# Optimization experiments

Hardware: AMD Instinct MI355X
Metric: run time of the kernel (lower is better)

## Reference

```python
import jax, jax.numpy as jnp
import numpy as np

B, T, L, D = 512, 100, 256, 128
DEPTH = 8                 # perfect binary tree depth -> path length DEPTH+1
P = DEPTH + 1
N_PER_TREE = 2 * L - 1    # 511 nodes per tree (heap layout)
N_TOTAL = T * N_PER_TREE  # 51100 global nodes


def _build_paths():
    # Heap layout per tree: internal nodes 0..L-2, leaves L-1..2L-2.
    # Path for leaf l = chain of heap ancestors from root to leaf.
    local = np.zeros((L, P), dtype=np.int32)
    for l in range(L):
        node = L - 1 + l
        chain = []
        while True:
            chain.append(node)
            if node == 0:
                break
            node = (node - 1) // 2
        local[l] = np.array(chain[::-1], dtype=np.int32)
    offs = (np.arange(T, dtype=np.int32) * N_PER_TREE)[:, None, None]
    return local[None, :, :] + offs  # [T, L, P] global node ids


def setup_inputs() -> dict:
    key = jax.random.key(0)
    k1, k2, k3, k4, k5, k6 = jax.random.split(key, 6)
    paths = jnp.asarray(_build_paths())
    # GBDT multi-hot: exactly one activated leaf per tree per sample
    leaf = jax.random.randint(k1, (B, T), 0, L)
    cross = (jnp.zeros((B, T, L), jnp.float32)
             .at[jnp.arange(B)[:, None], jnp.arange(T)[None, :], leaf]
             .set(1.0)
             .reshape(B, T * L))
    s = 1.0 / float(np.sqrt(D))  # torch LSTM init range
    node_emb = jax.random.normal(k2, (N_TOTAL, D), jnp.float32) * 0.01
    w_ih = jax.random.uniform(k3, (4 * D, D), jnp.float32, -s, s)
    w_hh = jax.random.uniform(k4, (4 * D, D), jnp.float32, -s, s)
    b_ih = jax.random.uniform(k5, (4 * D,), jnp.float32, -s, s)
    b_hh = jax.random.uniform(k6, (4 * D,), jnp.float32, -s, s)
    return {"cross_features": cross, "node_emb": node_emb, "w_ih": w_ih,
            "w_hh": w_hh, "b_ih": b_ih, "b_hh": b_hh, "paths": paths}


def _lstm_last_h(x, w_ih, w_hh, b_ih, b_hh):
    # x: [S, P, D] -> final hidden state [S, D]; torch gate order i, f, g, o
    S = x.shape[0]
    d = w_hh.shape[1]
    bias = b_ih + b_hh

    def step(carry, x_t):
        h, c = carry
        g = x_t @ w_ih.T + h @ w_hh.T + bias          # [S, 4D]
        i, f, gg, o = jnp.split(g, 4, axis=-1)
        c = jax.nn.sigmoid(f) * c + jax.nn.sigmoid(i) * jnp.tanh(gg)
        h = jax.nn.sigmoid(o) * jnp.tanh(c)
        return (h, c), None

    h0 = jnp.zeros((S, d), x.dtype)
    (h, _), _ = jax.lax.scan(step, (h0, h0), jnp.swapaxes(x, 0, 1))
    return h


def reference(cross_features, node_emb, w_ih, w_hh, b_ih, b_hh, paths):
    t, l, p = paths.shape
    b = cross_features.shape[0]
    d = node_emb.shape[1]
    cf = cross_features.reshape(b, t, l)
    leaf = jnp.argmax(cf, axis=-1)                    # [B, T] activated leaf per tree
    active = jnp.any(cf > 0, axis=-1)                 # [B, T] tree has an activated leaf
    node_ids = paths[jnp.arange(t)[None, :], leaf]    # [B, T, P] root-to-leaf global ids
    x = node_emb[node_ids].reshape(b * t, p, d)       # batched path gather
    h = _lstm_last_h(x, w_ih, w_hh, b_ih, b_hh).reshape(b, t, d)
    return jnp.where(active[..., None], h, jnp.zeros((), h.dtype))
```

## Files before the change

kernel.cpp:

```cpp
#include <hip/hip_runtime.h>
#include <math.h>


#define B_N 512
#define T_N 100
#define L_N 256
#define D_N 128
#define NPT 511

typedef __attribute__((ext_vector_type(8))) short short8;
typedef __attribute__((ext_vector_type(4))) float f32x4;
typedef __attribute__((ext_vector_type(4))) unsigned short ushort4v;

__device__ __forceinline__ unsigned short f2bf(float f) {
    unsigned u = __float_as_uint(f);
    return (unsigned short)((u + 0x7FFFu + ((u >> 16) & 1u)) >> 16);
}
__device__ __forceinline__ float bf2f(unsigned short b) {
    return __uint_as_float(((unsigned)b) << 16);
}
__device__ __forceinline__ float fsigmoid(float x) {
    return __builtin_amdgcn_rcpf(1.f + __builtin_amdgcn_exp2f(-1.44269504f * x));
}
__device__ __forceinline__ float ftanh(float x) {
    return 1.f - 2.f * __builtin_amdgcn_rcpf(1.f + __builtin_amdgcn_exp2f(2.88539009f * x));
}

__global__ __launch_bounds__(256) void pack_kernel(const float* __restrict__ w_ih,
                                                   const float* __restrict__ w_hh,
                                                   const float* __restrict__ b_ih,
                                                   const float* __restrict__ b_hh,
                                                   unsigned short* __restrict__ Bhi,
                                                   unsigned short* __restrict__ Blo,
                                                   float* __restrict__ bias) {
    const int idx = blockIdx.x * 256 + threadIdx.x;
    const int k  = idx & 255;
    const int np = idx >> 8;
    const float val = (k < 128) ? w_ih[(size_t)np * 128 + k]
                                : w_hh[(size_t)np * 128 + (k - 128)];
    const unsigned short hi = f2bf(val);
    const int kb = k >> 5, krel = k & 31, quad = krel >> 3, e = krel & 7;
    const int tn = np >> 4, col = np & 15, lane = quad * 16 + col;
    Bhi[(((size_t)kb * 32 + tn) * 64 + lane) * 8 + e] = hi;
    if (kb >= 4) {
        const unsigned short lo = f2bf(val - bf2f(hi));
        Blo[((((size_t)kb - 4) * 32 + tn) * 64 + lane) * 8 + e] = lo;
    }
    if (k == 0) bias[np] = b_ih[np] + b_hh[np];
}

__global__ __launch_bounds__(512, 2) void tree_kernel(
    const float* __restrict__ node_emb,
    const unsigned short* __restrict__ Bhi,
    const unsigned short* __restrict__ Blo,
    const float* __restrict__ bias,
    float* __restrict__ h7g, float* __restrict__ c7g,
    float* __restrict__ h8)
{
    __shared__ float hbuf[2][16][132];
    __shared__ float cbuf[2][16][132];
    __shared__ unsigned short AhiF[8 * 2 * 512];
    __shared__ unsigned short AloF[4 * 2 * 512];

    const int t    = blockIdx.x >> 2;
    const int s    = blockIdx.x & 3;
    const int tid  = threadIdx.x;
    const int idx  = tid >> 6;
    const int lane = tid & 63;
    const int ml   = lane & 15;
    const int quad = lane >> 4;
    const int j    = idx * 16 + ml;

    const float bi = bias[j];
    const float bf = bias[128 + j];
    const float bg = bias[256 + j];
    const float bo = bias[384 + j];

    const short8* Bh8 = reinterpret_cast<const short8*>(Bhi);
    const short8* Bl8 = reinterpret_cast<const short8*>(Blo);
    const short8* Ah8 = reinterpret_cast<const short8*>(AhiF);
    const short8* Al8 = reinterpret_cast<const short8*>(AloF);

    short8 bhR[8][4], blR[4][4];
    #pragma unroll
    for (int kb = 0; kb < 8; ++kb)
        #pragma unroll
        for (int g = 0; g < 4; ++g)
            bhR[kb][g] = Bh8[(kb * 32 + g * 8 + idx) * 64 + lane];
    #pragma unroll
    for (int kb = 0; kb < 4; ++kb)
        #pragma unroll
        for (int g = 0; g < 4; ++g)
            blR[kb][g] = Bl8[(kb * 32 + g * 8 + idx) * 64 + lane];

    for (int d = 0; d <= 6; ++d) {
        const int Mrows = (d == 0) ? 1 : (d == 1) ? 2 : (1 << (d - 2));
        const int pbase = (d >= 2) ? (s << (d - 2)) : 0;
        const bool root = (d == 0);
        const int cur = d & 1, prv = cur ^ 1;

        #pragma unroll
        for (int h2 = 0; h2 < 2; ++h2) {
            const int r  = tid & 15;
            const int k4 = (tid >> 4) + h2 * 32;
            const int k  = k4 * 4;
            int p = r; if (p > Mrows - 1) p = Mrows - 1;
            float4 v;
            if (k < 128) {
                const int local = (1 << d) - 1 + pbase + p;
                v = *reinterpret_cast<const float4*>(
                        node_emb + (size_t)(t * NPT + local) * D_N + k);
            } else if (root) {
                v = make_float4(0.f, 0.f, 0.f, 0.f);
            } else {
                const int pr = (d == 2) ? (s >> 1) : (p >> 1);
                v = *reinterpret_cast<const float4*>(&hbuf[prv][pr][k - 128]);
            }
            const int kb = k >> 5, qk = (k & 31) >> 3, e0 = k & 4;
            const ushort4v hv = { f2bf(v.x), f2bf(v.y), f2bf(v.z), f2bf(v.w) };
            *reinterpret_cast<ushort4v*>(
                &AhiF[((kb * 2 + 0) * 64 + qk * 16 + r) * 8 + e0]) = hv;
            if (k >= 128) {
                const ushort4v lv = { f2bf(v.x - bf2f(hv.x)), f2bf(v.y - bf2f(hv.y)),
                                      f2bf(v.z - bf2f(hv.z)), f2bf(v.w - bf2f(hv.w)) };
                *reinterpret_cast<ushort4v*>(
                    &AloF[(((kb - 4) * 2 + 0) * 64 + qk * 16 + r) * 8 + e0]) = lv;
            }
        }
        __syncthreads();

        float cpre[4];
        #pragma unroll
        for (int rr = 0; rr < 4; ++rr) {
            int m = quad * 4 + rr;
            if (m > Mrows - 1) m = Mrows - 1;
            const int pr = (d == 2) ? (s >> 1) : (m >> 1);
            cpre[rr] = root ? 0.f : cbuf[prv][pr][j];
        }

        f32x4 acc[4];
        #pragma unroll
        for (int g = 0; g < 4; ++g) acc[g] = (f32x4)0.f;

        #pragma unroll
        for (int kb = 0; kb < 8; ++kb) {
            const short8 ah = Ah8[(kb * 2 + 0) * 64 + lane];
            short8 al;
            if (kb >= 4) al = Al8[((kb - 4) * 2 + 0) * 64 + lane];
            #pragma unroll
            for (int g = 0; g < 4; ++g) {
                acc[g] = __builtin_amdgcn_mfma_f32_16x16x32_bf16(
                    ah, bhR[kb][g], acc[g], 0, 0, 0);
                if (kb >= 4) {
                    acc[g] = __builtin_amdgcn_mfma_f32_16x16x32_bf16(
                        ah, blR[kb - 4][g], acc[g], 0, 0, 0);
                    acc[g] = __builtin_amdgcn_mfma_f32_16x16x32_bf16(
                        al, bhR[kb][g], acc[g], 0, 0, 0);
                }
            }
        }

        #pragma unroll
        for (int rr = 0; rr < 4; ++rr) {
            const int m = quad * 4 + rr;
            if (m < Mrows) {
                const float ig = fsigmoid(acc[0][rr] + bi);
                const float fg = fsigmoid(acc[1][rr] + bf);
                const float gv = ftanh(acc[2][rr] + bg);
                const float og = fsigmoid(acc[3][rr] + bo);
                const float cn = fg * cpre[rr] + ig * gv;
                const float hn = og * ftanh(cn);
                hbuf[cur][m][j] = hn;
                cbuf[cur][m][j] = cn;
            }
        }
        __syncthreads();
    }

    {
        #pragma unroll
        for (int h2 = 0; h2 < 4; ++h2) {
            const int r  = tid & 31;
            const int k4 = (tid >> 5) + h2 * 16;
            const int k  = k4 * 4;
            const int mt = r >> 4, mlr = r & 15;
            float4 v;
            if (k < 128) {
                const int local = 127 + s * 32 + r;
                v = *reinterpret_cast<const float4*>(
                        node_emb + (size_t)(t * NPT + local) * D_N + k);
            } else {
                v = *reinterpret_cast<const float4*>(&hbuf[0][r >> 1][k - 128]);
            }
            const int kb = k >> 5, qk = (k & 31) >> 3, e0 = k & 4;
            const ushort4v hv = { f2bf(v.x), f2bf(v.y), f2bf(v.z), f2bf(v.w) };
            *reinterpret_cast<ushort4v*>(
                &AhiF[((kb * 2 + mt) * 64 + qk * 16 + mlr) * 8 + e0]) = hv;
            if (k >= 128) {
                const ushort4v lv = { f2bf(v.x - bf2f(hv.x)), f2bf(v.y - bf2f(hv.y)),
                                      f2bf(v.z - bf2f(hv.z)), f2bf(v.w - bf2f(hv.w)) };
                *reinterpret_cast<ushort4v*>(
                    &AloF[(((kb - 4) * 2 + mt) * 64 + qk * 16 + mlr) * 8 + e0]) = lv;
            }
        }
        __syncthreads();

        #pragma unroll
        for (int mt = 0; mt < 2; ++mt) {
            float cpre[4];
            #pragma unroll
            for (int rr = 0; rr < 4; ++rr) {
                const int m = mt * 16 + quad * 4 + rr;
                cpre[rr] = cbuf[0][m >> 1][j];
            }
            f32x4 acc[4];
            #pragma unroll
            for (int g = 0; g < 4; ++g) acc[g] = (f32x4)0.f;
            #pragma unroll
            for (int kb = 0; kb < 8; ++kb) {
                const short8 ah = Ah8[(kb * 2 + mt) * 64 + lane];
                short8 al;
                if (kb >= 4) al = Al8[((kb - 4) * 2 + mt) * 64 + lane];
                #pragma unroll
                for (int g = 0; g < 4; ++g) {
                    acc[g] = __builtin_amdgcn_mfma_f32_16x16x32_bf16(
                        ah, bhR[kb][g], acc[g], 0, 0, 0);
                    if (kb >= 4) {
                        acc[g] = __builtin_amdgcn_mfma_f32_16x16x32_bf16(
                            ah, blR[kb - 4][g], acc[g], 0, 0, 0);
                        acc[g] = __builtin_amdgcn_mfma_f32_16x16x32_bf16(
                            al, bhR[kb][g], acc[g], 0, 0, 0);
                    }
                }
            }
            #pragma unroll
            for (int rr = 0; rr < 4; ++rr) {
                const int m = mt * 16 + quad * 4 + rr;
                const float ig = fsigmoid(acc[0][rr] + bi);
                const float fg = fsigmoid(acc[1][rr] + bf);
                const float gv = ftanh(acc[2][rr] + bg);
                const float og = fsigmoid(acc[3][rr] + bo);
                const float cn = fg * cpre[rr] + ig * gv;
                const float hn = og * ftanh(cn);
                const size_t row = (size_t)(blockIdx.x * 32 + m) * D_N + j;
                h7g[row] = hn;
                c7g[row] = cn;
            }
        }
        __syncthreads();
    }

    for (int pp = 0; pp < 2; ++pp) {
        #pragma unroll
        for (int h2 = 0; h2 < 4; ++h2) {
            const int r  = tid & 31;
            const int m2 = pp * 32 + r;
            const int k4 = (tid >> 5) + h2 * 16;
            const int k  = k4 * 4;
            const int mt = r >> 4, mlr = r & 15;
            float4 v;
            if (k < 128) {
                const int local = 255 + s * 64 + m2;
                v = *reinterpret_cast<const float4*>(
                        node_emb + (size_t)(t * NPT + local) * D_N + k);
            } else {
                v = *reinterpret_cast<const float4*>(
                        h7g + (size_t)(blockIdx.x * 32 + (m2 >> 1)) * D_N + (k - 128));
            }
            const int kb = k >> 5, qk = (k & 31) >> 3, e0 = k & 4;
            const ushort4v hv = { f2bf(v.x), f2bf(v.y), f2bf(v.z), f2bf(v.w) };
            *reinterpret_cast<ushort4v*>(
                &AhiF[((kb * 2 + mt) * 64 + qk * 16 + mlr) * 8 + e0]) = hv;
            if (k >= 128) {
                const ushort4v lv = { f2bf(v.x - bf2f(hv.x)), f2bf(v.y - bf2f(hv.y)),
                                      f2bf(v.z - bf2f(hv.z)), f2bf(v.w - bf2f(hv.w)) };
                *reinterpret_cast<ushort4v*>(
                    &AloF[(((kb - 4) * 2 + mt) * 64 + qk * 16 + mlr) * 8 + e0]) = lv;
            }
        }
        __syncthreads();

        #pragma unroll
        for (int mt = 0; mt < 2; ++mt) {
            float cpre[4];
            #pragma unroll
            for (int rr = 0; rr < 4; ++rr) {
                const int m2 = pp * 32 + mt * 16 + quad * 4 + rr;
                cpre[rr] = c7g[(size_t)(blockIdx.x * 32 + (m2 >> 1)) * D_N + j];
            }
            f32x4 acc[4];
            #pragma unroll
            for (int g = 0; g < 4; ++g) acc[g] = (f32x4)0.f;
            #pragma unroll
            for (int kb = 0; kb < 8; ++kb) {
                const short8 ah = Ah8[(kb * 2 + mt) * 64 + lane];
                short8 al;
                if (kb >= 4) al = Al8[((kb - 4) * 2 + mt) * 64 + lane];
                #pragma unroll
                for (int g = 0; g < 4; ++g) {
                    acc[g] = __builtin_amdgcn_mfma_f32_16x16x32_bf16(
                        ah, bhR[kb][g], acc[g], 0, 0, 0);
                    if (kb >= 4) {
                        acc[g] = __builtin_amdgcn_mfma_f32_16x16x32_bf16(
                            ah, blR[kb - 4][g], acc[g], 0, 0, 0);
                        acc[g] = __builtin_amdgcn_mfma_f32_16x16x32_bf16(
                            al, bhR[kb][g], acc[g], 0, 0, 0);
                    }
                }
            }
            #pragma unroll
            for (int rr = 0; rr < 4; ++rr) {
                const int m2 = pp * 32 + mt * 16 + quad * 4 + rr;
                const float ig = fsigmoid(acc[0][rr] + bi);
                const float fg = fsigmoid(acc[1][rr] + bf);
                const float gv = ftanh(acc[2][rr] + bg);
                const float og = fsigmoid(acc[3][rr] + bo);
                const float cn = fg * cpre[rr] + ig * gv;
                const float hn = og * ftanh(cn);
                h8[(size_t)((t << 8) + s * 64 + m2) * D_N + j] = hn;
            }
        }
        __syncthreads();
    }
}

__global__ __launch_bounds__(256) void gather_kernel(const float* __restrict__ cross,
                                                     const float* __restrict__ h8,
                                                     float* __restrict__ out) {
    const int bt   = blockIdx.x * 4 + (threadIdx.x >> 6);
    const int lane = threadIdx.x & 63;
    const int t    = bt % T_N;
    const float4 v = reinterpret_cast<const float4*>(cross + (size_t)bt * L_N)[lane];
    int idx = -1;
    if      (v.x > 0.f) idx = lane * 4 + 0;
    else if (v.y > 0.f) idx = lane * 4 + 1;
    else if (v.z > 0.f) idx = lane * 4 + 2;
    else if (v.w > 0.f) idx = lane * 4 + 3;
    const unsigned long long m = __ballot(idx >= 0);
    int lf = -1;
    if (m != 0ULL) {
        const int first = __builtin_ctzll(m);
        lf = __shfl(idx, first);
    }
    float2 o = make_float2(0.f, 0.f);
    if (lf >= 0)
        o = reinterpret_cast<const float2*>(h8 + (size_t)(t * L_N + lf) * D_N)[lane];
    reinterpret_cast<float2*>(out + (size_t)bt * D_N)[lane] = o;
}

extern "C" void kernel_launch(void* const* d_in, const int* in_sizes, int n_in,
                              void* d_out, int out_size, void* d_ws, size_t ws_size,
                              hipStream_t stream) {
    const float* cross    = (const float*)d_in[0];
    const float* node_emb = (const float*)d_in[1];
    const float* w_ih     = (const float*)d_in[2];
    const float* w_hh     = (const float*)d_in[3];
    const float* b_ih     = (const float*)d_in[4];
    const float* b_hh     = (const float*)d_in[5];
    float* out = (float*)d_out;
    float* ws  = (float*)d_ws;

    float* h8   = ws;
    float* h7g  = h8 + (size_t)25600 * D_N;
    float* c7g  = h7g + (size_t)12800 * D_N;
    float* bias = c7g + (size_t)12800 * D_N;
    unsigned short* Bhi = (unsigned short*)(bias + 512);
    unsigned short* Blo = Bhi + 131072;

    pack_kernel<<<512, 256, 0, stream>>>(w_ih, w_hh, b_ih, b_hh, Bhi, Blo, bias);

    tree_kernel<<<4 * T_N, 512, 0, stream>>>(node_emb, Bhi, Blo, bias,
                                             h7g, c7g, h8);

    gather_kernel<<<(B_N * T_N) / 4, 256, 0, stream>>>(cross, h8, out);
}
```

Baseline: 188.7 us.

## Split tree LSTM into trunk kernel plus per-level GEMM kernels for leaf levels

```diff
diff --git a/kernel.cpp b/kernel.cpp
--- a/kernel.cpp
+++ b/kernel.cpp
@@ -49,27 +49,26 @@
     if (k == 0) bias[np] = b_ih[np] + b_hh[np];
 }
 
-__global__ __launch_bounds__(512, 2) void tree_kernel(
+__global__ __launch_bounds__(512, 4) void trunk_kernel(
     const float* __restrict__ node_emb,
     const unsigned short* __restrict__ Bhi,
     const unsigned short* __restrict__ Blo,
     const float* __restrict__ bias,
-    float* __restrict__ h7g, float* __restrict__ c7g,
-    float* __restrict__ h8)
+    float* __restrict__ h6g, float* __restrict__ c6g)
 {
-    __shared__ float hbuf[2][16][132];
-    __shared__ float cbuf[2][16][132];
+    __shared__ float hbuf[32][132];
+    __shared__ float cbuf[32][132];
     __shared__ unsigned short AhiF[8 * 2 * 512];
     __shared__ unsigned short AloF[4 * 2 * 512];
 
-    const int t    = blockIdx.x >> 2;
-    const int s    = blockIdx.x & 3;
+    const int t    = blockIdx.x >> 1;
+    const int s    = blockIdx.x & 1;
     const int tid  = threadIdx.x;
-    const int idx  = tid >> 6;
+    const int widx = tid >> 6;
     const int lane = tid & 63;
     const int ml   = lane & 15;
     const int quad = lane >> 4;
-    const int j    = idx * 16 + ml;
+    const int j    = widx * 16 + ml;
 
     const float bi = bias[j];
     const float bf = bias[128 + j];
@@ -81,118 +80,38 @@
     const short8* Ah8 = reinterpret_cast<const short8*>(AhiF);
     const short8* Al8 = reinterpret_cast<const short8*>(AloF);
 
-    short8 bhR[8][4], blR[4][4];
-    #pragma unroll
-    for (int kb = 0; kb < 8; ++kb)
-        #pragma unroll
-        for (int g = 0; g < 4; ++g)
-            bhR[kb][g] = Bh8[(kb * 32 + g * 8 + idx) * 64 + lane];
-    #pragma unroll
-    for (int kb = 0; kb < 4; ++kb)
-        #pragma unroll
-        for (int g = 0; g < 4; ++g)
-            blR[kb][g] = Bl8[(kb * 32 + g * 8 + idx) * 64 + lane];
-
     for (int d = 0; d <= 6; ++d) {
-        const int Mrows = (d == 0) ? 1 : (d == 1) ? 2 : (1 << (d - 2));
-        const int pbase = (d >= 2) ? (s << (d - 2)) : 0;
-        const bool root = (d == 0);
-        const int cur = d & 1, prv = cur ^ 1;
-
-        #pragma unroll
-        for (int h2 = 0; h2 < 2; ++h2) {
-            const int r  = tid & 15;
-            const int k4 = (tid >> 4) + h2 * 32;
-            const int k  = k4 * 4;
-            int p = r; if (p > Mrows - 1) p = Mrows - 1;
+        const int rows = (d == 0) ? 1 : (1 << (d - 1));
+
+        float cpre[2][4];
+        #pragma unroll
+        for (int mt = 0; mt < 2; ++mt)
+            #pragma unroll
+            for (int rr = 0; rr < 4; ++rr) {
+                int m = mt * 16 + quad * 4 + rr;
+                if (m > rows - 1) m = rows - 1;
+                cpre[mt][rr] = (d == 0) ? 0.f : cbuf[m >> 1][j];
+            }
+
+        #pragma unroll
+        for (int h2 = 0; h2 < 4; ++h2) {
+            const int r  = tid >> 4;
+            const int kq = tid & 15;
+            const int k  = (kq + h2 * 16) * 4;
+            int p = r; if (p > rows - 1) p = rows - 1;
             float4 v;
             if (k < 128) {
-                const int local = (1 << d) - 1 + pbase + p;
+                const int pg   = (d == 0) ? 0 : ((s << (d - 1)) + p);
+                const int node = (1 << d) - 1 + pg;
                 v = *reinterpret_cast<const float4*>(
-                        node_emb + (size_t)(t * NPT + local) * D_N + k);
-            } else if (root) {
+                        node_emb + (size_t)(t * NPT + node) * D_N + k);
+            } else if (d == 0) {
                 v = make_float4(0.f, 0.f, 0.f, 0.f);
             } else {
-                const int pr = (d == 2) ? (s >> 1) : (p >> 1);
-                v = *reinterpret_cast<const float4*>(&hbuf[prv][pr][k - 128]);
+                v = *reinterpret_cast<const float4*>(&hbuf[p >> 1][k - 128]);
             }
             const int kb = k >> 5, qk = (k & 31) >> 3, e0 = k & 4;
-            const ushort4v hv = { f2bf(v.x), f2bf(v.y), f2bf(v.z), f2bf(v.w) };
-            *reinterpret_cast<ushort4v*>(
-                &AhiF[((kb * 2 + 0) * 64 + qk * 16 + r) * 8 + e0]) = hv;
-            if (k >= 128) {
-                const ushort4v lv = { f2bf(v.x - bf2f(hv.x)), f2bf(v.y - bf2f(hv.y)),
-                                      f2bf(v.z - bf2f(hv.z)), f2bf(v.w - bf2f(hv.w)) };
-                *reinterpret_cast<ushort4v*>(
-                    &AloF[(((kb - 4) * 2 + 0) * 64 + qk * 16 + r) * 8 + e0]) = lv;
-            }
-        }
-        __syncthreads();
-
-        float cpre[4];
-        #pragma unroll
-        for (int rr = 0; rr < 4; ++rr) {
-            int m = quad * 4 + rr;
-            if (m > Mrows - 1) m = Mrows - 1;
-            const int pr = (d == 2) ? (s >> 1) : (m >> 1);
-            cpre[rr] = root ? 0.f : cbuf[prv][pr][j];
-        }
-
-        f32x4 acc[4];
-        #pragma unroll
-        for (int g = 0; g < 4; ++g) acc[g] = (f32x4)0.f;
-
-        #pragma unroll
-        for (int kb = 0; kb < 8; ++kb) {
-            const short8 ah = Ah8[(kb * 2 + 0) * 64 + lane];
-            short8 al;
-            if (kb >= 4) al = Al8[((kb - 4) * 2 + 0) * 64 + lane];
-            #pragma unroll
-            for (int g = 0; g < 4; ++g) {
-                acc[g] = __builtin_amdgcn_mfma_f32_16x16x32_bf16(
-                    ah, bhR[kb][g], acc[g], 0, 0, 0);
-                if (kb >= 4) {
-                    acc[g] = __builtin_amdgcn_mfma_f32_16x16x32_bf16(
-                        ah, blR[kb - 4][g], acc[g], 0, 0, 0);
-                    acc[g] = __builtin_amdgcn_mfma_f32_16x16x32_bf16(
-                        al, bhR[kb][g], acc[g], 0, 0, 0);
-                }
-            }
-        }
-
-        #pragma unroll
-        for (int rr = 0; rr < 4; ++rr) {
-            const int m = quad * 4 + rr;
-            if (m < Mrows) {
-                const float ig = fsigmoid(acc[0][rr] + bi);
-                const float fg = fsigmoid(acc[1][rr] + bf);
-                const float gv = ftanh(acc[2][rr] + bg);
-                const float og = fsigmoid(acc[3][rr] + bo);
-                const float cn = fg * cpre[rr] + ig * gv;
-                const float hn = og * ftanh(cn);
-                hbuf[cur][m][j] = hn;
-                cbuf[cur][m][j] = cn;
-            }
-        }
-        __syncthreads();
-    }
-
-    {
-        #pragma unroll
-        for (int h2 = 0; h2 < 4; ++h2) {
-            const int r  = tid & 31;
-            const int k4 = (tid >> 5) + h2 * 16;
-            const int k  = k4 * 4;
             const int mt = r >> 4, mlr = r & 15;
-            float4 v;
-            if (k < 128) {
-                const int local = 127 + s * 32 + r;
-                v = *reinterpret_cast<const float4*>(
-                        node_emb + (size_t)(t * NPT + local) * D_N + k);
-            } else {
-                v = *reinterpret_cast<const float4*>(&hbuf[0][r >> 1][k - 128]);
-            }
-            const int kb = k >> 5, qk = (k & 31) >> 3, e0 = k & 4;
             const ushort4v hv = { f2bf(v.x), f2bf(v.y), f2bf(v.z), f2bf(v.w) };
             *reinterpret_cast<ushort4v*>(
                 &AhiF[((kb * 2 + mt) * 64 + qk * 16 + mlr) * 8 + e0]) = hv;
@@ -205,14 +124,8 @@
         }
         __syncthreads();
 
-        #pragma unroll
-        for (int mt = 0; mt < 2; ++mt) {
-            float cpre[4];
-            #pragma unroll
-            for (int rr = 0; rr < 4; ++rr) {
-                const int m = mt * 16 + quad * 4 + rr;
-                cpre[rr] = cbuf[0][m >> 1][j];
-            }
+        const int nmt = (rows > 16) ? 2 : 1;
+        for (int mt = 0; mt < nmt; ++mt) {
             f32x4 acc[4];
             #pragma unroll
             for (int g = 0; g < 4; ++g) acc[g] = (f32x4)0.f;
@@ -223,105 +136,182 @@
                 if (kb >= 4) al = Al8[((kb - 4) * 2 + mt) * 64 + lane];
                 #pragma unroll
                 for (int g = 0; g < 4; ++g) {
-                    acc[g] = __builtin_amdgcn_mfma_f32_16x16x32_bf16(
-                        ah, bhR[kb][g], acc[g], 0, 0, 0);
+                    const short8 bh = Bh8[(kb * 32 + g * 8 + widx) * 64 + lane];
+                    acc[g] = __builtin_amdgcn_mfma_f32_16x16x32_bf16(ah, bh, acc[g], 0, 0, 0);
                     if (kb >= 4) {
-                        acc[g] = __builtin_amdgcn_mfma_f32_16x16x32_bf16(
-                            ah, blR[kb - 4][g], acc[g], 0, 0, 0);
-                        acc[g] = __builtin_amdgcn_mfma_f32_16x16x32_bf16(
-                            al, bhR[kb][g], acc[g], 0, 0, 0);
+                        const short8 bl = Bl8[((kb - 4) * 32 + g * 8 + widx) * 64 + lane];
+                        acc[g] = __builtin_amdgcn_mfma_f32_16x16x32_bf16(ah, bl, acc[g], 0, 0, 0);
+                        acc[g] = __builtin_amdgcn_mfma_f32_16x16x32_bf16(al, bh, acc[g], 0, 0, 0);
                     }
                 }
             }
             #pragma unroll
             for (int rr = 0; rr < 4; ++rr) {
                 const int m = mt * 16 + quad * 4 + rr;
-                const float ig = fsigmoid(acc[0][rr] + bi);
-                const float fg = fsigmoid(acc[1][rr] + bf);
-                const float gv = ftanh(acc[2][rr] + bg);
-                const float og = fsigmoid(acc[3][rr] + bo);
-                const float cn = fg * cpre[rr] + ig * gv;
-                const float hn = og * ftanh(cn);
-                const size_t row = (size_t)(blockIdx.x * 32 + m) * D_N + j;
-                h7g[row] = hn;
-                c7g[row] = cn;
-            }
-        }
-        __syncthreads();
-    }
-
-    for (int pp = 0; pp < 2; ++pp) {
-        #pragma unroll
-        for (int h2 = 0; h2 < 4; ++h2) {
-            const int r  = tid & 31;
-            const int m2 = pp * 32 + r;
-            const int k4 = (tid >> 5) + h2 * 16;
-            const int k  = k4 * 4;
-            const int mt = r >> 4, mlr = r & 15;
-            float4 v;
-            if (k < 128) {
-                const int local = 255 + s * 64 + m2;
-                v = *reinterpret_cast<const float4*>(
-                        node_emb + (size_t)(t * NPT + local) * D_N + k);
-            } else {
-                v = *reinterpret_cast<const float4*>(
-                        h7g + (size_t)(blockIdx.x * 32 + (m2 >> 1)) * D_N + (k - 128));
-            }
-            const int kb = k >> 5, qk = (k & 31) >> 3, e0 = k & 4;
-            const ushort4v hv = { f2bf(v.x), f2bf(v.y), f2bf(v.z), f2bf(v.w) };
-            *reinterpret_cast<ushort4v*>(
-                &AhiF[((kb * 2 + mt) * 64 + qk * 16 + mlr) * 8 + e0]) = hv;
-            if (k >= 128) {
-                const ushort4v lv = { f2bf(v.x - bf2f(hv.x)), f2bf(v.y - bf2f(hv.y)),
-                                      f2bf(v.z - bf2f(hv.z)), f2bf(v.w - bf2f(hv.w)) };
-                *reinterpret_cast<ushort4v*>(
-                    &AloF[(((kb - 4) * 2 + mt) * 64 + qk * 16 + mlr) * 8 + e0]) = lv;
-            }
-        }
-        __syncthreads();
-
-        #pragma unroll
-        for (int mt = 0; mt < 2; ++mt) {
-            float cpre[4];
-            #pragma unroll
-            for (int rr = 0; rr < 4; ++rr) {
-                const int m2 = pp * 32 + mt * 16 + quad * 4 + rr;
-                cpre[rr] = c7g[(size_t)(blockIdx.x * 32 + (m2 >> 1)) * D_N + j];
-            }
-            f32x4 acc[4];
-            #pragma unroll
-            for (int g = 0; g < 4; ++g) acc[g] = (f32x4)0.f;
-            #pragma unroll
-            for (int kb = 0; kb < 8; ++kb) {
-                const short8 ah = Ah8[(kb * 2 + mt) * 64 + lane];
-                short8 al;
-                if (kb >= 4) al = Al8[((kb - 4) * 2 + mt) * 64 + lane];
-                #pragma unroll
-                for (int g = 0; g < 4; ++g) {
-                    acc[g] = __builtin_amdgcn_mfma_f32_16x16x32_bf16(
-                        ah, bhR[kb][g], acc[g], 0, 0, 0);
-                    if (kb >= 4) {
-                        acc[g] = __builtin_amdgcn_mfma_f32_16x16x32_bf16(
-                            ah, blR[kb - 4][g], acc[g], 0, 0, 0);
-                        acc[g] = __builtin_amdgcn_mfma_f32_16x16x32_bf16(
-                            al, bhR[kb][g], acc[g], 0, 0, 0);
+                if (m < rows) {
+                    const float ig = fsigmoid(acc[0][rr] + bi);
+                    const float fg = fsigmoid(acc[1][rr] + bf);
+                    const float gv = ftanh(acc[2][rr] + bg);
+                    const float og = fsigmoid(acc[3][rr] + bo);
+                    const float cn = fg * cpre[mt][rr] + ig * gv;
+                    const float hn = og * ftanh(cn);
+                    hbuf[m][j] = hn;
+                    cbuf[m][j] = cn;
+                    if (d == 6) {
+                        const size_t row = (size_t)(t * 64 + s * 32 + m) * D_N + j;
+                        h6g[row] = hn;
+                        c6g[row] = cn;
                     }
                 }
             }
-            #pragma unroll
-            for (int rr = 0; rr < 4; ++rr) {
-                const int m2 = pp * 32 + mt * 16 + quad * 4 + rr;
-                const float ig = fsigmoid(acc[0][rr] + bi);
-                const float fg = fsigmoid(acc[1][rr] + bf);
-                const float gv = ftanh(acc[2][rr] + bg);
-                const float og = fsigmoid(acc[3][rr] + bo);
-                const float cn = fg * cpre[rr] + ig * gv;
-                const float hn = og * ftanh(cn);
-                h8[(size_t)((t << 8) + s * 64 + m2) * D_N + j] = hn;
-            }
         }
         __syncthreads();
     }
+}
+
+__global__ __launch_bounds__(512, 4) void gemm_kernel(
+    const float* __restrict__ node_emb,
+    const unsigned short* __restrict__ Bhi,
+    const unsigned short* __restrict__ Blo,
+    const float* __restrict__ bias,
+    const float* __restrict__ hsrc,
+    const float* __restrict__ csrc,
+    float* __restrict__ hdst,
+    float* __restrict__ cdst,
+    const int rpt_sh,
+    const int node_off)
+{
+    __shared__ unsigned short AhiF[8 * 2 * 512];
+    __shared__ unsigned short AloF[4 * 2 * 512];
+    __shared__ int4 BL[2048];
+
+    const int tid  = threadIdx.x;
+    const int widx = tid >> 6;
+    const int lane = tid & 63;
+    const int ml   = lane & 15;
+    const int quad = lane >> 4;
+    const int j    = widx * 16 + ml;
+
+    const int b0 = blockIdx.x * 32;
+    const int t  = b0 >> rpt_sh;
+    const int q0 = b0 & ((1 << rpt_sh) - 1);
+    const size_t nbase = (size_t)(t * NPT + node_off) * D_N;
+    const size_t pbase = ((size_t)t << (rpt_sh - 1)) * D_N;
+
+    const float bi = bias[j];
+    const float bf = bias[128 + j];
+    const float bg = bias[256 + j];
+    const float bo = bias[384 + j];
+
+    const short8* Ah8 = reinterpret_cast<const short8*>(AhiF);
+    const short8* Al8 = reinterpret_cast<const short8*>(AloF);
+    const short8* BL8 = reinterpret_cast<const short8*>(BL);
+
+    #pragma unroll
+    for (int h2 = 0; h2 < 4; ++h2) {
+        const int r  = tid >> 4;
+        const int kq = tid & 15;
+        const int k  = (kq + h2 * 16) * 4;
+        const int q  = q0 + r;
+        float4 v;
+        if (k < 128)
+            v = *reinterpret_cast<const float4*>(node_emb + nbase + (size_t)q * D_N + k);
+        else
+            v = *reinterpret_cast<const float4*>(hsrc + pbase + (size_t)(q >> 1) * D_N + (k - 128));
+        const int kb = k >> 5, qk = (k & 31) >> 3, e0 = k & 4;
+        const int mt = r >> 4, mlr = r & 15;
+        const ushort4v hv = { f2bf(v.x), f2bf(v.y), f2bf(v.z), f2bf(v.w) };
+        *reinterpret_cast<ushort4v*>(
+            &AhiF[((kb * 2 + mt) * 64 + qk * 16 + mlr) * 8 + e0]) = hv;
+        if (k >= 128) {
+            const ushort4v lv = { f2bf(v.x - bf2f(hv.x)), f2bf(v.y - bf2f(hv.y)),
+                                  f2bf(v.z - bf2f(hv.z)), f2bf(v.w - bf2f(hv.w)) };
+            *reinterpret_cast<ushort4v*>(
+                &AloF[(((kb - 4) * 2 + mt) * 64 + qk * 16 + mlr) * 8 + e0]) = lv;
+        }
+    }
+
+    float cpre[2][4];
+    #pragma unroll
+    for (int mt = 0; mt < 2; ++mt)
+        #pragma unroll
+        for (int rr = 0; rr < 4; ++rr) {
+            const int q = q0 + mt * 16 + quad * 4 + rr;
+            cpre[mt][rr] = csrc[pbase + (size_t)(q >> 1) * D_N + j];
+        }
+    __syncthreads();
+
+    f32x4 acc[2][4];
+    #pragma unroll
+    for (int mt = 0; mt < 2; ++mt)
+        #pragma unroll
+        for (int g = 0; g < 4; ++g) acc[mt][g] = (f32x4)0.f;
+
+    #pragma unroll
+    for (int kb = 0; kb < 8; ++kb) {
+        {
+            const int4* src = reinterpret_cast<const int4*>(Bhi) + kb * 2048;
+            #pragma unroll
+            for (int c = 0; c < 4; ++c) BL[tid + c * 512] = src[tid + c * 512];
+        }
+        __syncthreads();
+        {
+            short8 bh[4];
+            #pragma unroll
+            for (int g = 0; g < 4; ++g) bh[g] = BL8[(g * 8 + widx) * 64 + lane];
+            #pragma unroll
+            for (int mt = 0; mt < 2; ++mt) {
+                const short8 ah = Ah8[(kb * 2 + mt) * 64 + lane];
+                #pragma unroll
+                for (int g = 0; g < 4; ++g)
+                    acc[mt][g] = __builtin_amdgcn_mfma_f32_16x16x32_bf16(ah, bh[g], acc[mt][g], 0, 0, 0);
+                if (kb >= 4) {
+                    const short8 al = Al8[((kb - 4) * 2 + mt) * 64 + lane];
+                    #pragma unroll
+                    for (int g = 0; g < 4; ++g)
+                        acc[mt][g] = __builtin_amdgcn_mfma_f32_16x16x32_bf16(al, bh[g], acc[mt][g], 0, 0, 0);
+                }
+            }
+        }
+        __syncthreads();
+        if (kb >= 4) {
+            {
+                const int4* src = reinterpret_cast<const int4*>(Blo) + (kb - 4) * 2048;
+                #pragma unroll
+                for (int c = 0; c < 4; ++c) BL[tid + c * 512] = src[tid + c * 512];
+            }
+            __syncthreads();
+            {
+                short8 bl[4];
+                #pragma unroll
+                for (int g = 0; g < 4; ++g) bl[g] = BL8[(g * 8 + widx) * 64 + lane];
+                #pragma unroll
+                for (int mt = 0; mt < 2; ++mt) {
+                    const short8 ah = Ah8[(kb * 2 + mt) * 64 + lane];
+                    #pragma unroll
+                    for (int g = 0; g < 4; ++g)
+                        acc[mt][g] = __builtin_amdgcn_mfma_f32_16x16x32_bf16(ah, bl[g], acc[mt][g], 0, 0, 0);
+                }
+            }
+            __syncthreads();
+        }
+    }
+
+    #pragma unroll
+    for (int mt = 0; mt < 2; ++mt)
+        #pragma unroll
+        for (int rr = 0; rr < 4; ++rr) {
+            const int m  = mt * 16 + quad * 4 + rr;
+            const float ig = fsigmoid(acc[mt][0][rr] + bi);
+            const float fg = fsigmoid(acc[mt][1][rr] + bf);
+            const float gv = ftanh(acc[mt][2][rr] + bg);
+            const float og = fsigmoid(acc[mt][3][rr] + bo);
+            const float cn = fg * cpre[mt][rr] + ig * gv;
+            const float hn = og * ftanh(cn);
+            const size_t row = (size_t)(b0 + m) * D_N + j;
+            hdst[row] = hn;
+            if (cdst) cdst[row] = cn;
+        }
 }
 
 __global__ __launch_bounds__(256) void gather_kernel(const float* __restrict__ cross,
@@ -366,11 +356,18 @@
     float* bias = c7g + (size_t)12800 * D_N;
     unsigned short* Bhi = (unsigned short*)(bias + 512);
     unsigned short* Blo = Bhi + 131072;
+    float* c6g = h8;
+    float* h6g = h8 + (size_t)6400 * D_N;
 
     pack_kernel<<<512, 256, 0, stream>>>(w_ih, w_hh, b_ih, b_hh, Bhi, Blo, bias);
 
-    tree_kernel<<<4 * T_N, 512, 0, stream>>>(node_emb, Bhi, Blo, bias,
-                                             h7g, c7g, h8);
+    trunk_kernel<<<2 * T_N, 512, 0, stream>>>(node_emb, Bhi, Blo, bias, h6g, c6g);
+
+    gemm_kernel<<<400, 512, 0, stream>>>(node_emb, Bhi, Blo, bias,
+                                         h6g, c6g, h7g, c7g, 7, 127);
+
+    gemm_kernel<<<800, 512, 0, stream>>>(node_emb, Bhi, Blo, bias,
+                                         h7g, c7g, h8, nullptr, 8, 255);
 
     gather_kernel<<<(B_N * T_N) / 4, 256, 0, stream>>>(cross, h8, out);
 }
```

Result: slower. 305.2 us (+61.7%).
